# Kernel optimization log

Measured on AMD Instinct MI355X. Metric: run time of the kernel, lower is better.

## Reference

```python
import jax, jax.numpy as jnp
import numpy as np

# module-level constants from the original repo
NUM_CLASSES = 4
CLASS_NONE = 0
RETINA_SIZE = 224.0

# loss weights (ContourLoss defaults)
POINT_W, ORIENT_W, CLASS_W, INTERSECT_W = 1.0, 0.5, 1.0, 0.1

B, S = 8, 2048


def setup_inputs() -> dict:
    key = jax.random.key(0)
    k1, k2, k3, k4, k5, k6, k7 = jax.random.split(key, 7)
    point_pred = jax.random.uniform(k1, (B, S, 2), jnp.float32) * RETINA_SIZE
    orient_pred = jax.random.normal(k2, (B, S, 2), jnp.float32)
    orient_pred = orient_pred / jnp.linalg.norm(orient_pred, axis=-1, keepdims=True)
    class_pred = jax.random.normal(k3, (B, S, NUM_CLASSES), jnp.float32)
    tgt_pts = jax.random.uniform(k4, (B, S, 2), jnp.float32) * RETINA_SIZE
    tgt_orient = jax.random.normal(k5, (B, S, 2), jnp.float32)
    tgt_orient = tgt_orient / jnp.linalg.norm(tgt_orient, axis=-1, keepdims=True)
    tgt_cls = jax.random.randint(k6, (B, S), 0, NUM_CLASSES).astype(jnp.float32)
    target_seq = jnp.concatenate([tgt_pts, tgt_orient, tgt_cls[..., None]], axis=-1)
    padding_mask = jax.random.bernoulli(k7, 0.15, (B, S))
    return {"point_pred": point_pred, "orient_pred": orient_pred,
            "class_pred": class_pred, "target_seq": target_seq,
            "padding_mask": padding_mask}


def _intersection_per_sample(pts, non_none):
    # pts: (S,2), non_none: (S,) bool.
    # Compact valid points to the front (stable), mirroring point_pred[b, valid_idx].
    order = jnp.argsort(jnp.logical_not(non_none), stable=True)
    pts_c = pts[order]                      # (S,2), first n rows valid
    n = non_none.sum()
    n_seg = n - 1
    starts, ends = pts_c[:-1], pts_c[1:]    # (S-1,2)
    M = S - 1
    ii = jnp.arange(M)[:, None]
    jj = jnp.arange(M)[None, :]
    mask = ((jj >= ii + 2) & (ii < n_seg) & (jj < n_seg)
            & ~((ii == 0) & (jj == n_seg - 1)) & (n >= 4))
    p1 = starts[:, None, :]; p2 = ends[:, None, :]   # segment i
    p3 = starts[None, :, :]; p4 = ends[None, :, :]   # segment j

    def cross(a, b, c):
        return ((b[..., 0] - a[..., 0]) * (c[..., 1] - a[..., 1])
                - (b[..., 1] - a[..., 1]) * (c[..., 0] - a[..., 0]))

    d1 = cross(p3, p4, p1)
    d2 = cross(p3, p4, p2)
    d3 = cross(p1, p2, p3)
    d4 = cross(p1, p2, p4)
    s = jax.nn.sigmoid(-d1 * d2 * 0.01) * jax.nn.sigmoid(-d3 * d4 * 0.01)
    return jnp.where(mask, s, 0.0).sum(), mask.sum()


def reference(point_pred, orient_pred, class_pred, target_seq, padding_mask):
    Bd, Sd, _ = class_pred.shape
    target_class = target_seq[:, :, 4].astype(jnp.int32)
    target_point = target_seq[:, :, :2]
    target_orient = target_seq[:, :, 2:4]
    valid = jnp.logical_not(padding_mask)
    valid_f = valid.astype(jnp.float32)

    # classification: cross entropy, masked mean over valid tokens
    logp = jax.nn.log_softmax(class_pred, axis=-1)
    cls = -jnp.take_along_axis(logp, target_class[..., None], axis=-1)[..., 0]
    cls_loss = (cls * valid_f).sum() / jnp.maximum(valid_f.sum(), 1.0)

    non_none = valid & (target_class != CLASS_NONE)
    nn_f = non_none.astype(jnp.float32)
    nn_denom = jnp.maximum(nn_f.sum(), 1.0)

    # point: SmoothL1 (beta=1) on normalized coords, mean over xy, masked mean
    d = (point_pred - target_point) / RETINA_SIZE
    ad = jnp.abs(d)
    sl1 = jnp.where(ad < 1.0, 0.5 * d * d, ad - 0.5).mean(axis=-1)
    pt_loss = (sl1 * nn_f).sum() / nn_denom

    # orientation: 1 - cosine similarity (orient_pred assumed L2-normalized)
    cos_sim = (orient_pred * target_orient).sum(axis=-1)
    orient_loss = ((1.0 - cos_sim) * nn_f).sum() / nn_denom

    # intersection penalty over non-adjacent segment pairs, per sample
    sums, counts = jax.vmap(_intersection_per_sample)(point_pred, non_none)
    cnt = counts.sum()
    intersect_loss = jnp.where(cnt > 0, sums.sum() / jnp.maximum(cnt, 1).astype(jnp.float32), 0.0)

    total = (POINT_W * pt_loss + ORIENT_W * orient_loss
             + CLASS_W * cls_loss + INTERSECT_W * intersect_loss)
    return (total, pt_loss, orient_loss, cls_loss, intersect_loss)
```

## Files before the change

### kernel.cpp

```cpp
#include <hip/hip_runtime.h>

#define B 8
#define S 2048
#define NBPS 128
#define NBLK_INTER (B * NBPS)
#define NBLK_LOSS 64
#define NBLK_TOTAL (NBLK_INTER + NBLK_LOSS)
#define TPB 256


__global__ __launch_bounds__(TPB) void mega_kernel(
    const float2* __restrict__ point_pred,
    const float2* __restrict__ orient_pred,
    const float4* __restrict__ class_pred,
    const float*  __restrict__ target_seq,
    const int*    __restrict__ padding_mask,
    int*   __restrict__ n_buf,
    float* __restrict__ partial,
    float* __restrict__ acc2)
{
    __shared__ float2 sp[S];
    __shared__ float red[TPB / 64][5];
    __shared__ int wsum[TPB / 64], woff[TPB / 64], nTot;

    const int blk = blockIdx.x;
    const int tid = threadIdx.x;
    const int lane = tid & 63, wv = tid >> 6;

    if (blk < NBLK_INTER) {
        const int b = blk >> 7;
        const int iblk = blk & (NBPS - 1);
        const int base = b * S;
        const int e0 = tid * 8;

        const int4* pm4 = (const int4*)(padding_mask + base + e0);
        const int4 ma = pm4[0], mb = pm4[1];
        float t4v[8];
        #pragma unroll
        for (int k = 0; k < 8; ++k)
            t4v[k] = target_seq[(base + e0 + k) * 5 + 4];
        const float4* pq4 = (const float4*)(point_pred + base + e0);
        const float4 pa = pq4[0], pb = pq4[1], pc = pq4[2], pd = pq4[3];
        float2 p[8];
        p[0] = make_float2(pa.x, pa.y); p[1] = make_float2(pa.z, pa.w);
        p[2] = make_float2(pb.x, pb.y); p[3] = make_float2(pb.z, pb.w);
        p[4] = make_float2(pc.x, pc.y); p[5] = make_float2(pc.z, pc.w);
        p[6] = make_float2(pd.x, pd.y); p[7] = make_float2(pd.z, pd.w);
        int f[8];
        f[0] = (ma.x == 0 && (int)t4v[0] != 0) ? 1 : 0;
        f[1] = (ma.y == 0 && (int)t4v[1] != 0) ? 1 : 0;
        f[2] = (ma.z == 0 && (int)t4v[2] != 0) ? 1 : 0;
        f[3] = (ma.w == 0 && (int)t4v[3] != 0) ? 1 : 0;
        f[4] = (mb.x == 0 && (int)t4v[4] != 0) ? 1 : 0;
        f[5] = (mb.y == 0 && (int)t4v[5] != 0) ? 1 : 0;
        f[6] = (mb.z == 0 && (int)t4v[6] != 0) ? 1 : 0;
        f[7] = (mb.w == 0 && (int)t4v[7] != 0) ? 1 : 0;

        const int c = f[0]+f[1]+f[2]+f[3]+f[4]+f[5]+f[6]+f[7];
        int inc = c;
        #pragma unroll
        for (int off = 1; off < 64; off <<= 1) {
            int u = __shfl_up(inc, (unsigned)off, 64);
            if (lane >= off) inc += u;
        }
        if (lane == 63) wsum[wv] = inc;
        __syncthreads();
        if (tid == 0) {
            int run = 0;
            #pragma unroll
            for (int w = 0; w < TPB / 64; ++w) { woff[w] = run; run += wsum[w]; }
            nTot = run;
        }
        __syncthreads();
        int pos = woff[wv] + inc - c;
        #pragma unroll
        for (int k = 0; k < 8; ++k) { if (f[k]) sp[pos++] = p[k]; }
        __syncthreads();

        const int n = nTot;
        if (iblk == 0 && tid == 0) n_buf[b] = n;

        float local = 0.f;
        if (n >= 4) {
            const int n_seg = n - 1;
            for (int i = iblk; i < n_seg - 2; i += NBPS) {
                const float2 q1 = sp[i], q2 = sp[i + 1];
                const float e12x = q2.x - q1.x, e12y = q2.y - q1.y;
                const int jmax = (i == 0) ? n_seg - 1 : n_seg;
                for (int j = i + 2 + tid; j < jmax; j += TPB) {
                    const float2 q3 = sp[j], q4 = sp[j + 1];
                    const float e34x = q4.x - q3.x, e34y = q4.y - q3.y;
                    const float ce = e12x * e34y - e12y * e34x;
                    const float rx = q1.x - q3.x, ry = q1.y - q3.y;
                    const float d1 = e34x * ry - e34y * rx;
                    const float d3 = e12y * rx - e12x * ry;
                    const float d2 = d1 - ce;
                    const float d4 = d3 + ce;
                    const float ea = __expf(d1 * d2 * 0.01f);
                    const float eb = __expf(d3 * d4 * 0.01f);
                    local += __builtin_amdgcn_rcpf((1.f + ea) * (1.f + eb));
                }
            }
        }
        #pragma unroll
        for (int off = 32; off > 0; off >>= 1)
            local += __shfl_down(local, (unsigned)off, 64);
        if (lane == 0) red[wv][0] = local;
        __syncthreads();
        if (tid == 0)
            partial[blk] = red[0][0] + red[1][0] + red[2][0] + red[3][0];
    } else {
        const int idx = (blk - NBLK_INTER) * TPB + tid;
        const bool valid = (padding_mask[idx] == 0);
        const float t4 = target_seq[idx * 5 + 4];
        const int tc = (int)t4;
        const bool nn = valid && (tc != 0);
        float cls_acc = 0.f, pt_acc = 0.f, or_acc = 0.f, v_acc = 0.f, nn_acc = 0.f;
        if (valid) {
            const float4 cl = class_pred[idx];
            const float m = fmaxf(fmaxf(cl.x, cl.y), fmaxf(cl.z, cl.w));
            const float lse = m + logf(expf(cl.x - m) + expf(cl.y - m) +
                                       expf(cl.z - m) + expf(cl.w - m));
            const float ct = (tc == 0) ? cl.x : (tc == 1) ? cl.y : (tc == 2) ? cl.z : cl.w;
            cls_acc = lse - ct;
            v_acc = 1.f;
        }
        if (nn) {
            const float2 pp = point_pred[idx];
            const float tx = target_seq[idx * 5 + 0];
            const float ty = target_seq[idx * 5 + 1];
            const float dx = (pp.x - tx) * (1.0f / 224.0f);
            const float dy = (pp.y - ty) * (1.0f / 224.0f);
            const float adx = fabsf(dx), ady = fabsf(dy);
            const float l0 = (adx < 1.f) ? 0.5f * dx * dx : adx - 0.5f;
            const float l1 = (ady < 1.f) ? 0.5f * dy * dy : ady - 0.5f;
            pt_acc = 0.5f * (l0 + l1);
            const float2 op = orient_pred[idx];
            const float ox = target_seq[idx * 5 + 2];
            const float oy = target_seq[idx * 5 + 3];
            or_acc = 1.f - (op.x * ox + op.y * oy);
            nn_acc = 1.f;
        }
        #pragma unroll
        for (int off = 32; off > 0; off >>= 1) {
            cls_acc += __shfl_down(cls_acc, (unsigned)off, 64);
            pt_acc  += __shfl_down(pt_acc,  (unsigned)off, 64);
            or_acc  += __shfl_down(or_acc,  (unsigned)off, 64);
            v_acc   += __shfl_down(v_acc,   (unsigned)off, 64);
            nn_acc  += __shfl_down(nn_acc,  (unsigned)off, 64);
        }
        if (lane == 0) {
            red[wv][0] = cls_acc; red[wv][1] = pt_acc; red[wv][2] = or_acc;
            red[wv][3] = v_acc;   red[wv][4] = nn_acc;
        }
        __syncthreads();
        if (tid == 0) {
            float* dst = acc2 + (blk - NBLK_INTER) * 5;
            #pragma unroll
            for (int c5 = 0; c5 < 5; ++c5)
                dst[c5] = red[0][c5] + red[1][c5] + red[2][c5] + red[3][c5];
        }
    }
}

__global__ __launch_bounds__(TPB) void finalize_kernel(
    const float* __restrict__ acc2,
    const int* __restrict__ n_buf,
    const float* __restrict__ partial,
    float* __restrict__ out)
{
    __shared__ float red[TPB / 64][5];
    const int tid = threadIdx.x;
    const int lane = tid & 63, wv = tid >> 6;

    float s = partial[tid] + partial[tid + 256] + partial[tid + 512] + partial[tid + 768];
    #pragma unroll
    for (int off = 32; off > 0; off >>= 1)
        s += __shfl_down(s, (unsigned)off, 64);
    if (lane == 0) red[wv][0] = s;
    __syncthreads();
    const float inter_sum = red[0][0] + red[1][0] + red[2][0] + red[3][0];
    __syncthreads();

    float a0 = 0, a1 = 0, a2 = 0, a3 = 0, a4 = 0;
    if (tid < NBLK_LOSS) {
        a0 = acc2[tid * 5 + 0]; a1 = acc2[tid * 5 + 1]; a2 = acc2[tid * 5 + 2];
        a3 = acc2[tid * 5 + 3]; a4 = acc2[tid * 5 + 4];
    }
    #pragma unroll
    for (int off = 32; off > 0; off >>= 1) {
        a0 += __shfl_down(a0, (unsigned)off, 64);
        a1 += __shfl_down(a1, (unsigned)off, 64);
        a2 += __shfl_down(a2, (unsigned)off, 64);
        a3 += __shfl_down(a3, (unsigned)off, 64);
        a4 += __shfl_down(a4, (unsigned)off, 64);
    }
    if (lane == 0) {
        red[wv][0] = a0; red[wv][1] = a1; red[wv][2] = a2;
        red[wv][3] = a3; red[wv][4] = a4;
    }
    __syncthreads();
    if (tid == 0) {
        const float cls_sum = red[0][0] + red[1][0] + red[2][0] + red[3][0];
        const float pt_sum  = red[0][1] + red[1][1] + red[2][1] + red[3][1];
        const float or_sum  = red[0][2] + red[1][2] + red[2][2] + red[3][2];
        const float vcnt    = red[0][3] + red[1][3] + red[2][3] + red[3][3];
        const float nncnt   = red[0][4] + red[1][4] + red[2][4] + red[3][4];
        long long cnt = 0;
        #pragma unroll
        for (int b2 = 0; b2 < B; ++b2) {
            const int n = n_buf[b2];
            if (n >= 4) {
                const long long ns = n - 1;
                cnt += (ns - 1) * (ns - 2) / 2 - 1;
            }
        }
        const float cls_loss = cls_sum / fmaxf(vcnt, 1.f);
        const float pt_loss = pt_sum / fmaxf(nncnt, 1.f);
        const float orient_loss = or_sum / fmaxf(nncnt, 1.f);
        const float intersect_loss = (cnt > 0) ? inter_sum / (float)cnt : 0.f;
        out[0] = 1.0f * pt_loss + 0.5f * orient_loss +
                 1.0f * cls_loss + 0.1f * intersect_loss;
        out[1] = pt_loss;
        out[2] = orient_loss;
        out[3] = cls_loss;
        out[4] = intersect_loss;
    }
}

extern "C" void kernel_launch(void* const* d_in, const int* in_sizes, int n_in,
                              void* d_out, int out_size, void* d_ws, size_t ws_size,
                              hipStream_t stream) {
    (void)in_sizes; (void)n_in; (void)out_size; (void)ws_size;
    const float2* point_pred  = (const float2*)d_in[0];
    const float2* orient_pred = (const float2*)d_in[1];
    const float4* class_pred  = (const float4*)d_in[2];
    const float*  target_seq  = (const float*)d_in[3];
    const int*    padding_mask = (const int*)d_in[4];

    int*   n_buf   = (int*)d_ws;
    float* partial = (float*)((char*)d_ws + 64);
    float* acc2    = (float*)((char*)d_ws + 4224);

    mega_kernel<<<NBLK_TOTAL, TPB, 0, stream>>>(point_pred, orient_pred,
                                                class_pred, target_seq,
                                                padding_mask,
                                                n_buf, partial, acc2);
    finalize_kernel<<<1, TPB, 0, stream>>>(acc2, n_buf, partial, (float*)d_out);
}
```

Measured before the change: 20.13 us.

## Merge loss blocks into intersection blocks and halve blocks per sample

Removes the separate per-element loss blocks and has each intersection block also compute the pointwise losses for a 32-element slice, with the wave-0 partials written in channel-major layout. Blocks per sample drop from 128 to 64, which doubles the i-rows each block handles. Target class values are now read with vectorized float4 loads of the whole target rows instead of strided scalar reads. The finalize kernel shrinks to one wave with vectorized partial loads. This cuts launch and prologue overhead but reduces parallelism in the O(n^2) intersection loop.

```diff
diff --git a/kernel.cpp b/kernel.cpp
--- a/kernel.cpp
+++ b/kernel.cpp
@@ -2,11 +2,10 @@
 
 #define B 8
 #define S 2048
-#define NBPS 128
-#define NBLK_INTER (B * NBPS)
-#define NBLK_LOSS 64
-#define NBLK_TOTAL (NBLK_INTER + NBLK_LOSS)
+#define NBPS 64
+#define NBLK (B * NBPS)
 #define TPB 256
+#define LPB (S / NBPS)
 
 
 __global__ __launch_bounds__(TPB) void mega_kernel(
@@ -20,192 +19,176 @@
     float* __restrict__ acc2)
 {
     __shared__ float2 sp[S];
-    __shared__ float red[TPB / 64][5];
+    __shared__ float red[TPB / 64][1];
     __shared__ int wsum[TPB / 64], woff[TPB / 64], nTot;
 
     const int blk = blockIdx.x;
     const int tid = threadIdx.x;
     const int lane = tid & 63, wv = tid >> 6;
-
-    if (blk < NBLK_INTER) {
-        const int b = blk >> 7;
-        const int iblk = blk & (NBPS - 1);
-        const int base = b * S;
-        const int e0 = tid * 8;
-
-        const int4* pm4 = (const int4*)(padding_mask + base + e0);
-        const int4 ma = pm4[0], mb = pm4[1];
-        float t4v[8];
-        #pragma unroll
-        for (int k = 0; k < 8; ++k)
-            t4v[k] = target_seq[(base + e0 + k) * 5 + 4];
-        const float4* pq4 = (const float4*)(point_pred + base + e0);
-        const float4 pa = pq4[0], pb = pq4[1], pc = pq4[2], pd = pq4[3];
-        float2 p[8];
-        p[0] = make_float2(pa.x, pa.y); p[1] = make_float2(pa.z, pa.w);
-        p[2] = make_float2(pb.x, pb.y); p[3] = make_float2(pb.z, pb.w);
-        p[4] = make_float2(pc.x, pc.y); p[5] = make_float2(pc.z, pc.w);
-        p[6] = make_float2(pd.x, pd.y); p[7] = make_float2(pd.z, pd.w);
-        int f[8];
-        f[0] = (ma.x == 0 && (int)t4v[0] != 0) ? 1 : 0;
-        f[1] = (ma.y == 0 && (int)t4v[1] != 0) ? 1 : 0;
-        f[2] = (ma.z == 0 && (int)t4v[2] != 0) ? 1 : 0;
-        f[3] = (ma.w == 0 && (int)t4v[3] != 0) ? 1 : 0;
-        f[4] = (mb.x == 0 && (int)t4v[4] != 0) ? 1 : 0;
-        f[5] = (mb.y == 0 && (int)t4v[5] != 0) ? 1 : 0;
-        f[6] = (mb.z == 0 && (int)t4v[6] != 0) ? 1 : 0;
-        f[7] = (mb.w == 0 && (int)t4v[7] != 0) ? 1 : 0;
-
-        const int c = f[0]+f[1]+f[2]+f[3]+f[4]+f[5]+f[6]+f[7];
-        int inc = c;
-        #pragma unroll
-        for (int off = 1; off < 64; off <<= 1) {
-            int u = __shfl_up(inc, (unsigned)off, 64);
-            if (lane >= off) inc += u;
-        }
-        if (lane == 63) wsum[wv] = inc;
-        __syncthreads();
-        if (tid == 0) {
-            int run = 0;
-            #pragma unroll
-            for (int w = 0; w < TPB / 64; ++w) { woff[w] = run; run += wsum[w]; }
-            nTot = run;
-        }
-        __syncthreads();
-        int pos = woff[wv] + inc - c;
-        #pragma unroll
-        for (int k = 0; k < 8; ++k) { if (f[k]) sp[pos++] = p[k]; }
-        __syncthreads();
-
-        const int n = nTot;
-        if (iblk == 0 && tid == 0) n_buf[b] = n;
-
-        float local = 0.f;
-        if (n >= 4) {
-            const int n_seg = n - 1;
-            for (int i = iblk; i < n_seg - 2; i += NBPS) {
-                const float2 q1 = sp[i], q2 = sp[i + 1];
-                const float e12x = q2.x - q1.x, e12y = q2.y - q1.y;
-                const int jmax = (i == 0) ? n_seg - 1 : n_seg;
-                for (int j = i + 2 + tid; j < jmax; j += TPB) {
-                    const float2 q3 = sp[j], q4 = sp[j + 1];
-                    const float e34x = q4.x - q3.x, e34y = q4.y - q3.y;
-                    const float ce = e12x * e34y - e12y * e34x;
-                    const float rx = q1.x - q3.x, ry = q1.y - q3.y;
-                    const float d1 = e34x * ry - e34y * rx;
-                    const float d3 = e12y * rx - e12x * ry;
-                    const float d2 = d1 - ce;
-                    const float d4 = d3 + ce;
-                    const float ea = __expf(d1 * d2 * 0.01f);
-                    const float eb = __expf(d3 * d4 * 0.01f);
-                    local += __builtin_amdgcn_rcpf((1.f + ea) * (1.f + eb));
-                }
-            }
-        }
-        #pragma unroll
-        for (int off = 32; off > 0; off >>= 1)
-            local += __shfl_down(local, (unsigned)off, 64);
-        if (lane == 0) red[wv][0] = local;
-        __syncthreads();
-        if (tid == 0)
-            partial[blk] = red[0][0] + red[1][0] + red[2][0] + red[3][0];
-    } else {
-        const int idx = (blk - NBLK_INTER) * TPB + tid;
+    const int b = blk >> 6;
+    const int iblk = blk & (NBPS - 1);
+    const int base = b * S;
+    const int e0 = tid * 8;
+
+    const int4* pm4 = (const int4*)(padding_mask + base + e0);
+    const int4 ma = pm4[0], mb = pm4[1];
+    const float4* tr4 = (const float4*)(target_seq + (size_t)(base + e0) * 5);
+    float4 tq[10];
+    #pragma unroll
+    for (int k = 0; k < 10; ++k) tq[k] = tr4[k];
+    float t4v[8];
+    t4v[0] = tq[1].x; t4v[1] = tq[2].y; t4v[2] = tq[3].z; t4v[3] = tq[4].w;
+    t4v[4] = tq[6].x; t4v[5] = tq[7].y; t4v[6] = tq[8].z; t4v[7] = tq[9].w;
+    const float4* pq4 = (const float4*)(point_pred + base + e0);
+    const float4 pa = pq4[0], pb = pq4[1], pc = pq4[2], pd = pq4[3];
+    float2 p[8];
+    p[0] = make_float2(pa.x, pa.y); p[1] = make_float2(pa.z, pa.w);
+    p[2] = make_float2(pb.x, pb.y); p[3] = make_float2(pb.z, pb.w);
+    p[4] = make_float2(pc.x, pc.y); p[5] = make_float2(pc.z, pc.w);
+    p[6] = make_float2(pd.x, pd.y); p[7] = make_float2(pd.z, pd.w);
+    int f[8];
+    f[0] = (ma.x == 0 && (int)t4v[0] != 0) ? 1 : 0;
+    f[1] = (ma.y == 0 && (int)t4v[1] != 0) ? 1 : 0;
+    f[2] = (ma.z == 0 && (int)t4v[2] != 0) ? 1 : 0;
+    f[3] = (ma.w == 0 && (int)t4v[3] != 0) ? 1 : 0;
+    f[4] = (mb.x == 0 && (int)t4v[4] != 0) ? 1 : 0;
+    f[5] = (mb.y == 0 && (int)t4v[5] != 0) ? 1 : 0;
+    f[6] = (mb.z == 0 && (int)t4v[6] != 0) ? 1 : 0;
+    f[7] = (mb.w == 0 && (int)t4v[7] != 0) ? 1 : 0;
+
+    float cls_a = 0.f, pt_a = 0.f, or_a = 0.f, v_a = 0.f, nn_a = 0.f;
+    if (tid < LPB) {
+        const int idx = base + iblk * LPB + tid;
         const bool valid = (padding_mask[idx] == 0);
-        const float t4 = target_seq[idx * 5 + 4];
+        const float* row = target_seq + (size_t)idx * 5;
+        const float t4 = row[4];
         const int tc = (int)t4;
         const bool nn = valid && (tc != 0);
-        float cls_acc = 0.f, pt_acc = 0.f, or_acc = 0.f, v_acc = 0.f, nn_acc = 0.f;
         if (valid) {
             const float4 cl = class_pred[idx];
             const float m = fmaxf(fmaxf(cl.x, cl.y), fmaxf(cl.z, cl.w));
             const float lse = m + logf(expf(cl.x - m) + expf(cl.y - m) +
                                        expf(cl.z - m) + expf(cl.w - m));
             const float ct = (tc == 0) ? cl.x : (tc == 1) ? cl.y : (tc == 2) ? cl.z : cl.w;
-            cls_acc = lse - ct;
-            v_acc = 1.f;
+            cls_a = lse - ct;
+            v_a = 1.f;
         }
         if (nn) {
             const float2 pp = point_pred[idx];
-            const float tx = target_seq[idx * 5 + 0];
-            const float ty = target_seq[idx * 5 + 1];
-            const float dx = (pp.x - tx) * (1.0f / 224.0f);
-            const float dy = (pp.y - ty) * (1.0f / 224.0f);
+            const float dx = (pp.x - row[0]) * (1.0f / 224.0f);
+            const float dy = (pp.y - row[1]) * (1.0f / 224.0f);
             const float adx = fabsf(dx), ady = fabsf(dy);
             const float l0 = (adx < 1.f) ? 0.5f * dx * dx : adx - 0.5f;
             const float l1 = (ady < 1.f) ? 0.5f * dy * dy : ady - 0.5f;
-            pt_acc = 0.5f * (l0 + l1);
+            pt_a = 0.5f * (l0 + l1);
             const float2 op = orient_pred[idx];
-            const float ox = target_seq[idx * 5 + 2];
-            const float oy = target_seq[idx * 5 + 3];
-            or_acc = 1.f - (op.x * ox + op.y * oy);
-            nn_acc = 1.f;
-        }
+            or_a = 1.f - (op.x * row[2] + op.y * row[3]);
+            nn_a = 1.f;
+        }
+    }
+    if (wv == 0) {
         #pragma unroll
         for (int off = 32; off > 0; off >>= 1) {
-            cls_acc += __shfl_down(cls_acc, (unsigned)off, 64);
-            pt_acc  += __shfl_down(pt_acc,  (unsigned)off, 64);
-            or_acc  += __shfl_down(or_acc,  (unsigned)off, 64);
-            v_acc   += __shfl_down(v_acc,   (unsigned)off, 64);
-            nn_acc  += __shfl_down(nn_acc,  (unsigned)off, 64);
+            cls_a += __shfl_down(cls_a, (unsigned)off, 64);
+            pt_a  += __shfl_down(pt_a,  (unsigned)off, 64);
+            or_a  += __shfl_down(or_a,  (unsigned)off, 64);
+            v_a   += __shfl_down(v_a,   (unsigned)off, 64);
+            nn_a  += __shfl_down(nn_a,  (unsigned)off, 64);
         }
         if (lane == 0) {
-            red[wv][0] = cls_acc; red[wv][1] = pt_acc; red[wv][2] = or_acc;
-            red[wv][3] = v_acc;   red[wv][4] = nn_acc;
-        }
-        __syncthreads();
-        if (tid == 0) {
-            float* dst = acc2 + (blk - NBLK_INTER) * 5;
-            #pragma unroll
-            for (int c5 = 0; c5 < 5; ++c5)
-                dst[c5] = red[0][c5] + red[1][c5] + red[2][c5] + red[3][c5];
-        }
-    }
+            acc2[0 * NBLK + blk] = cls_a;
+            acc2[1 * NBLK + blk] = pt_a;
+            acc2[2 * NBLK + blk] = or_a;
+            acc2[3 * NBLK + blk] = v_a;
+            acc2[4 * NBLK + blk] = nn_a;
+        }
+    }
+
+    const int c = f[0]+f[1]+f[2]+f[3]+f[4]+f[5]+f[6]+f[7];
+    int inc = c;
+    #pragma unroll
+    for (int off = 1; off < 64; off <<= 1) {
+        int u = __shfl_up(inc, (unsigned)off, 64);
+        if (lane >= off) inc += u;
+    }
+    if (lane == 63) wsum[wv] = inc;
+    __syncthreads();
+    if (tid == 0) {
+        int run = 0;
+        #pragma unroll
+        for (int w = 0; w < TPB / 64; ++w) { woff[w] = run; run += wsum[w]; }
+        nTot = run;
+    }
+    __syncthreads();
+    int pos = woff[wv] + inc - c;
+    #pragma unroll
+    for (int k = 0; k < 8; ++k) { if (f[k]) sp[pos++] = p[k]; }
+    __syncthreads();
+
+    const int n = nTot;
+    if (iblk == 0 && tid == 0) n_buf[b] = n;
+
+    float local = 0.f;
+    if (n >= 4) {
+        const int n_seg = n - 1;
+        for (int i = iblk; i < n_seg - 2; i += NBPS) {
+            const float2 q1 = sp[i], q2 = sp[i + 1];
+            const float e12x = q2.x - q1.x, e12y = q2.y - q1.y;
+            const int jmax = (i == 0) ? n_seg - 1 : n_seg;
+            for (int j = i + 2 + tid; j < jmax; j += TPB) {
+                const float2 q3 = sp[j], q4 = sp[j + 1];
+                const float e34x = q4.x - q3.x, e34y = q4.y - q3.y;
+                const float ce = e12x * e34y - e12y * e34x;
+                const float rx = q1.x - q3.x, ry = q1.y - q3.y;
+                const float d1 = e34x * ry - e34y * rx;
+                const float d3 = e12y * rx - e12x * ry;
+                const float d2 = d1 - ce;
+                const float d4 = d3 + ce;
+                const float ea = __expf(d1 * d2 * 0.01f);
+                const float eb = __expf(d3 * d4 * 0.01f);
+                local += __builtin_amdgcn_rcpf((1.f + ea) * (1.f + eb));
+            }
+        }
+    }
+    #pragma unroll
+    for (int off = 32; off > 0; off >>= 1)
+        local += __shfl_down(local, (unsigned)off, 64);
+    if (lane == 0) red[wv][0] = local;
+    __syncthreads();
+    if (tid == 0)
+        partial[blk] = red[0][0] + red[1][0] + red[2][0] + red[3][0];
 }
 
-__global__ __launch_bounds__(TPB) void finalize_kernel(
+__global__ __launch_bounds__(64) void finalize_kernel(
     const float* __restrict__ acc2,
     const int* __restrict__ n_buf,
     const float* __restrict__ partial,
     float* __restrict__ out)
 {
-    __shared__ float red[TPB / 64][5];
-    const int tid = threadIdx.x;
-    const int lane = tid & 63, wv = tid >> 6;
-
-    float s = partial[tid] + partial[tid + 256] + partial[tid + 512] + partial[tid + 768];
-    #pragma unroll
-    for (int off = 32; off > 0; off >>= 1)
+    const int lane = threadIdx.x;
+
+    const float4* p4 = (const float4*)partial;
+    const float4 u = p4[lane * 2], v = p4[lane * 2 + 1];
+    float s = (u.x + u.y) + (u.z + u.w) + (v.x + v.y) + (v.z + v.w);
+
+    float a[5];
+    #pragma unroll
+    for (int ch = 0; ch < 5; ++ch) {
+        const float4* c4 = (const float4*)(acc2 + ch * NBLK);
+        const float4 x = c4[lane * 2], y = c4[lane * 2 + 1];
+        a[ch] = (x.x + x.y) + (x.z + x.w) + (y.x + y.y) + (y.z + y.w);
+    }
+
+    #pragma unroll
+    for (int off = 32; off > 0; off >>= 1) {
         s += __shfl_down(s, (unsigned)off, 64);
-    if (lane == 0) red[wv][0] = s;
-    __syncthreads();
-    const float inter_sum = red[0][0] + red[1][0] + red[2][0] + red[3][0];
-    __syncthreads();
-
-    float a0 = 0, a1 = 0, a2 = 0, a3 = 0, a4 = 0;
-    if (tid < NBLK_LOSS) {
-        a0 = acc2[tid * 5 + 0]; a1 = acc2[tid * 5 + 1]; a2 = acc2[tid * 5 + 2];
-        a3 = acc2[tid * 5 + 3]; a4 = acc2[tid * 5 + 4];
-    }
-    #pragma unroll
-    for (int off = 32; off > 0; off >>= 1) {
-        a0 += __shfl_down(a0, (unsigned)off, 64);
-        a1 += __shfl_down(a1, (unsigned)off, 64);
-        a2 += __shfl_down(a2, (unsigned)off, 64);
-        a3 += __shfl_down(a3, (unsigned)off, 64);
-        a4 += __shfl_down(a4, (unsigned)off, 64);
-    }
+        #pragma unroll
+        for (int ch = 0; ch < 5; ++ch)
+            a[ch] += __shfl_down(a[ch], (unsigned)off, 64);
+    }
+
     if (lane == 0) {
-        red[wv][0] = a0; red[wv][1] = a1; red[wv][2] = a2;
-        red[wv][3] = a3; red[wv][4] = a4;
-    }
-    __syncthreads();
-    if (tid == 0) {
-        const float cls_sum = red[0][0] + red[1][0] + red[2][0] + red[3][0];
-        const float pt_sum  = red[0][1] + red[1][1] + red[2][1] + red[3][1];
-        const float or_sum  = red[0][2] + red[1][2] + red[2][2] + red[3][2];
-        const float vcnt    = red[0][3] + red[1][3] + red[2][3] + red[3][3];
-        const float nncnt   = red[0][4] + red[1][4] + red[2][4] + red[3][4];
+        const float inter_sum = s;
         long long cnt = 0;
         #pragma unroll
         for (int b2 = 0; b2 < B; ++b2) {
@@ -215,9 +198,9 @@
                 cnt += (ns - 1) * (ns - 2) / 2 - 1;
             }
         }
-        const float cls_loss = cls_sum / fmaxf(vcnt, 1.f);
-        const float pt_loss = pt_sum / fmaxf(nncnt, 1.f);
-        const float orient_loss = or_sum / fmaxf(nncnt, 1.f);
+        const float cls_loss = a[0] / fmaxf(a[3], 1.f);
+        const float pt_loss = a[1] / fmaxf(a[4], 1.f);
+        const float orient_loss = a[2] / fmaxf(a[4], 1.f);
         const float intersect_loss = (cnt > 0) ? inter_sum / (float)cnt : 0.f;
         out[0] = 1.0f * pt_loss + 0.5f * orient_loss +
                  1.0f * cls_loss + 0.1f * intersect_loss;
@@ -240,11 +223,10 @@
 
     int*   n_buf   = (int*)d_ws;
     float* partial = (float*)((char*)d_ws + 64);
-    float* acc2    = (float*)((char*)d_ws + 4224);
-
-    mega_kernel<<<NBLK_TOTAL, TPB, 0, stream>>>(point_pred, orient_pred,
-                                                class_pred, target_seq,
-                                                padding_mask,
-                                                n_buf, partial, acc2);
-    finalize_kernel<<<1, TPB, 0, stream>>>(acc2, n_buf, partial, (float*)d_out);
+    float* acc2    = (float*)((char*)d_ws + 2176);
+
+    mega_kernel<<<NBLK, TPB, 0, stream>>>(point_pred, orient_pred, class_pred,
+                                          target_seq, padding_mask,
+                                          n_buf, partial, acc2);
+    finalize_kernel<<<1, 64, 0, stream>>>(acc2, n_buf, partial, (float*)d_out);
 }
```

After: 22.20 us. +10.3%, slower.
